# Kernel optimization log

Hardware: AMD Instinct MI355X
Metric: run time of the kernel (lower is better)

The kernel has to match this reference:

```python
import jax, jax.numpy as jnp
import numpy as np

DIM = 192
HEADS = 4
EMBED = 48


def setup_inputs() -> dict:
    key = jax.random.key(0)
    ks = jax.random.split(key, 8)
    b, c, h, w = 8, DIM, 128, 128
    x = jax.random.normal(ks[0], (b, c, h, w), dtype=jnp.float32)
    prior = jax.random.normal(ks[1], (b, 1, EMBED * 4), dtype=jnp.float32)
    # learned params (bias=False)
    w_qkv = jax.random.normal(ks[2], (3 * c, c), dtype=jnp.float32) * (1.0 / np.sqrt(c))
    w_dw = jax.random.normal(ks[3], (3 * c, 1, 3, 3), dtype=jnp.float32) * (1.0 / 3.0)
    w_proj = jax.random.normal(ks[4], (c, c), dtype=jnp.float32) * (1.0 / np.sqrt(c))
    w_kernel = jax.random.normal(ks[5], (2 * c, EMBED * 4), dtype=jnp.float32) * (1.0 / np.sqrt(EMBED * 4))
    temperature = jnp.ones((HEADS, 1, 1), dtype=jnp.float32)
    return {"x": x, "prior": prior, "w_qkv": w_qkv, "w_dw": w_dw,
            "w_proj": w_proj, "w_kernel": w_kernel, "temperature": temperature}


def _mdta(x, prior, w_qkv, w_dw, w_proj, w_kernel, temperature):
    b, c, h, w = x.shape
    # prior modulation: Linear(4*embed -> 2*dim), broadcast over (h,w)
    kv = jnp.einsum('blf,of->blo', prior, w_kernel)[:, 0]        # (b, 2c)
    kv1, kv2 = kv[:, :c], kv[:, c:]
    x = x * kv1[:, :, None, None] + kv2[:, :, None, None]
    # 1x1 conv -> depthwise 3x3 conv
    qkv = jnp.einsum('bchw,oc->bohw', x, w_qkv)                   # (b, 3c, h, w)
    qkv = jax.lax.conv_general_dilated(
        qkv, w_dw, window_strides=(1, 1), padding='SAME',
        dimension_numbers=('NCHW', 'OIHW', 'NCHW'), feature_group_count=3 * c)
    q, k, v = jnp.split(qkv, 3, axis=1)
    ch = c // HEADS
    def heads(t):  # (b, c, h, w) -> (b, head, ch, h*w)
        return t.reshape(b, HEADS, ch, h * w)
    q, k, v = heads(q), heads(k), heads(v)
    # L2 normalize over the (h w) reduction axis
    q = q / jnp.linalg.norm(q, axis=-1, keepdims=True).clip(1e-12)
    k = k / jnp.linalg.norm(k, axis=-1, keepdims=True).clip(1e-12)
    attn = jnp.einsum('bhcn,bhdn->bhcd', q, k) * temperature      # (b, head, ch, ch)
    attn = jax.nn.softmax(attn, axis=-1)
    out = jnp.einsum('bhcd,bhdn->bhcn', attn, v).reshape(b, c, h, w)
    return jnp.einsum('bchw,oc->bohw', out, w_proj)


def reference(x, prior, w_qkv, w_dw, w_proj, w_kernel, temperature):
    return _mdta(x, prior, w_qkv, w_dw, w_proj, w_kernel, temperature)
```

## Files before the change

kernel.cpp:

```cpp
#include <hip/hip_runtime.h>
#include <hip/hip_bf16.h>
#include <stdint.h>

typedef float f32x4 __attribute__((ext_vector_type(4)));
typedef __bf16 bf16x8 __attribute__((ext_vector_type(8)));
typedef __bf16 bf16x2 __attribute__((ext_vector_type(2)));

#define NB 8
#define NC 192
#define NO 576
#define NH 128
#define NWID 128
#define NSP 16384
#define NHEADS 4
#define NCH 48

#define OFF_KV    0u
#define OFF_SSQ   12288u
#define OFF_S     24576u
#define OFF_WB    319488u
#define OFF_M     540672u
#define OFF_QKV2  1130496u
#define OFF_QKV1  152125440u

__device__ __forceinline__ void g2l16(const void* g, void* l) {
    __builtin_amdgcn_global_load_lds((const __attribute__((address_space(1))) void*)g,
                                     (__attribute__((address_space(3))) void*)l, 16, 0, 0);
}

__global__ void k_kv(const float* __restrict__ prior, const float* __restrict__ w_kernel,
                     float* __restrict__ kv, float* __restrict__ zbase) {
    int t = blockIdx.x * 256 + threadIdx.x;
    for (int i = t; i < 76800; i += 3072) zbase[i] = 0.f;
    if (t >= NB * 384) return;
    int b = t / 384, j = t % 384;
    const float* p = prior + b * NC;
    const float* wk = w_kernel + j * NC;
    float s = 0.f;
    for (int f = 0; f < NC; ++f) s += p[f] * wk[f];
    kv[t] = s;
}

__global__ void k_wcast(const float* __restrict__ w_qkv, __bf16* __restrict__ Wb) {
    int t = blockIdx.x * 256 + threadIdx.x;
    if (t < NO * NC) Wb[t] = (__bf16)w_qkv[t];
}

__global__ __launch_bounds__(256, 2) void k_qkv(const float* __restrict__ x, const float* __restrict__ kv,
                                                const __bf16* __restrict__ Wb, __bf16* __restrict__ qkv1) {
    __shared__ __align__(16) char lds[73728];
    int b = blockIdx.y, n0 = blockIdx.x * 128;
    int t = threadIdx.x;
#pragma unroll
    for (int i = 0; i < 6; ++i) {
        int s = i * 256 + t;
        int r = s / 24, c = s % 24, g = c ^ ((r >> 2) & 7);
        g2l16(Wb + (size_t)r * NC + g * 8, lds + 49152 + s * 16);
    }
    const float* xb = x + (size_t)b * NC * NSP + n0;
    const float* kvb = kv + b * 384;
#pragma unroll 4
    for (int p = 0; p < 24; ++p) {
        int id = p * 256 + t;
        int c = id >> 5, n4 = (id & 31) << 2;
        f32x4 v = *reinterpret_cast<const f32x4*>(xb + (size_t)c * NSP + n4);
        float k1 = kvb[c], k2 = kvb[192 + c];
        int chi = (c >> 3) ^ ((n4 >> 2) & 7);
        int base = chi * 16 + (c & 7) * 2;
#pragma unroll
        for (int j = 0; j < 4; ++j)
            *reinterpret_cast<__bf16*>((char*)lds + (n4 + j) * 384 + base) = (__bf16)(v[j] * k1 + k2);
    }
    asm volatile("s_waitcnt vmcnt(0)" ::: "memory");
    __syncthreads();
    int w = t >> 6, l = t & 63, lr = l & 15, lg = l >> 4;
    bf16x8 bgf[6][2];
#pragma unroll
    for (int ks = 0; ks < 6; ++ks) {
        int c16 = ks * 4 + lg;
#pragma unroll
        for (int nf = 0; nf < 2; ++nf) {
            int r = w * 32 + nf * 16 + lr;
            bgf[ks][nf] = *reinterpret_cast<const bf16x8*>(lds + r * 384 + ((c16 ^ ((r >> 2) & 7)) << 4));
        }
    }
    for (int ot = 0; ot < 9; ++ot) {
        f32x4 acc[4][2] = {};
#pragma unroll
        for (int ks = 0; ks < 6; ++ks) {
            int c16 = ks * 4 + lg;
            bf16x8 a[4];
#pragma unroll
            for (int mf = 0; mf < 4; ++mf) {
                int r = mf * 16 + lr;
                a[mf] = *reinterpret_cast<const bf16x8*>(lds + 49152 + r * 384 + ((c16 ^ ((r >> 2) & 7)) << 4));
            }
#pragma unroll
            for (int mf = 0; mf < 4; ++mf)
#pragma unroll
                for (int nf = 0; nf < 2; ++nf)
                    acc[mf][nf] = __builtin_amdgcn_mfma_f32_16x16x32_bf16(a[mf], bgf[ks][nf], acc[mf][nf], 0, 0, 0);
        }
        __syncthreads();
        if (ot < 8) {
            const __bf16* asrc = Wb + (size_t)(ot + 1) * 64 * NC;
#pragma unroll
            for (int i = 0; i < 6; ++i) {
                int s = i * 256 + t;
                int r = s / 24, c = s % 24, g = c ^ ((r >> 2) & 7);
                g2l16(asrc + (size_t)r * NC + g * 8, lds + 49152 + s * 16);
            }
        }
        int o0 = ot * 64;
#pragma unroll
        for (int mf = 0; mf < 4; ++mf)
#pragma unroll
            for (int rr = 0; rr < 4; ++rr) {
                int orow = o0 + mf * 16 + lg * 4 + rr;
#pragma unroll
                for (int nf = 0; nf < 2; ++nf)
                    qkv1[(size_t)(b * NO + orow) * NSP + n0 + w * 32 + nf * 16 + lr] = (__bf16)acc[mf][nf][rr];
            }
        if (ot < 8) {
            asm volatile("s_waitcnt vmcnt(32)" ::: "memory");
            __syncthreads();
        }
    }
}

__global__ __launch_bounds__(256) void k_dw(const __bf16* __restrict__ qkv1, const float* __restrict__ w_dw,
                                            __bf16* __restrict__ qkv2, float* __restrict__ ssq) {
    int task = blockIdx.x * 4 + (threadIdx.x >> 6);
    int l = threadIdx.x & 63;
    int strip = task & 7;
    int bo = task >> 3;
    int o = bo % NO, b = bo / NO;
    const __bf16* src = qkv1 + (size_t)bo * NSP;
    __bf16* dst = qkv2 + (size_t)bo * NSP;
    float wd[9];
#pragma unroll
    for (int i = 0; i < 9; ++i) wd[i] = w_dw[o * 9 + i];
    int ys = strip * 16;
    float a0, b0, L0, R0, a1, b1, L1, R1, a2, b2, L2, R2;

#define LOADROW(Y, A, B, L_, R_) {                                            \
        bf16x2 p = {};                                                        \
        int y_ = (Y);                                                         \
        if (y_ >= 0 && y_ < NH) p = *reinterpret_cast<const bf16x2*>(src + y_ * NWID + 2 * l); \
        A = (float)p[0]; B = (float)p[1];                                     \
        L_ = __shfl(B, l - 1); R_ = __shfl(A, l + 1);                         \
        if (l == 0) L_ = 0.f;                                                 \
        if (l == 63) R_ = 0.f; }

    LOADROW(ys - 1, a0, b0, L0, R0)
    LOADROW(ys,     a1, b1, L1, R1)
    float ss = 0.f;
    bool qk = (o < 384);
#pragma unroll 4
    for (int i = 0; i < 16; ++i) {
        LOADROW(ys + i + 1, a2, b2, L2, R2)
        float oa = L0 * wd[0] + a0 * wd[1] + b0 * wd[2]
                 + L1 * wd[3] + a1 * wd[4] + b1 * wd[5]
                 + L2 * wd[6] + a2 * wd[7] + b2 * wd[8];
        float ob = a0 * wd[0] + b0 * wd[1] + R0 * wd[2]
                 + a1 * wd[3] + b1 * wd[4] + R1 * wd[5]
                 + a2 * wd[6] + b2 * wd[7] + R2 * wd[8];
        bf16x2 ov; ov[0] = (__bf16)oa; ov[1] = (__bf16)ob;
        *reinterpret_cast<bf16x2*>(dst + (ys + i) * NWID + 2 * l) = ov;
        if (qk) { float fa = (float)ov[0], fb = (float)ov[1]; ss += fa * fa + fb * fb; }
        a0 = a1; b0 = b1; L0 = L1; R0 = R1;
        a1 = a2; b1 = b2; L1 = L2; R1 = R2;
    }
#undef LOADROW
    if (qk) {
        for (int off = 32; off > 0; off >>= 1) ss += __shfl_down(ss, off);
        if (l == 0) atomicAdd(&ssq[b * 384 + o], ss);
    }
}

__global__ __launch_bounds__(256, 3) void k_sdot(const __bf16* __restrict__ qkv2, float* __restrict__ S) {
    __shared__ __align__(16) char lds[49152];
    int b = blockIdx.z, h = blockIdx.y, n0 = blockIdx.x * 512;
    int t = threadIdx.x;
    int w = t >> 6, l = t & 63, lr = l & 15, lg = l >> 4;
    const __bf16* qsrc = qkv2 + (size_t)(b * NO + h * NCH) * NSP + n0;
    const __bf16* ksrc = qkv2 + (size_t)(b * NO + 192 + h * NCH) * NSP + n0;
    f32x4 acc[3][3] = {};
    for (int pass = 0; pass < 2; ++pass) {
        if (pass) __syncthreads();
        int coff = pass * 256;
#pragma unroll
        for (int i = 0; i < 6; ++i) {
            int s = i * 256 + t;
            int r = s >> 5, c = s & 31, g = c ^ (r & 7);
            g2l16(qsrc + (size_t)r * NSP + coff + g * 8, lds + s * 16);
        }
#pragma unroll
        for (int i = 0; i < 6; ++i) {
            int s = i * 256 + t;
            int r = s >> 5, c = s & 31, g = c ^ (r & 7);
            g2l16(ksrc + (size_t)r * NSP + coff + g * 8, lds + 24576 + s * 16);
        }
        asm volatile("s_waitcnt vmcnt(0)" ::: "memory");
        __syncthreads();
#pragma unroll
        for (int j = 0; j < 2; ++j) {
            int c16 = (w * 2 + j) * 4 + lg;
            bf16x8 a[3], bb[3];
#pragma unroll
            for (int mf = 0; mf < 3; ++mf) {
                int r = mf * 16 + lr;
                a[mf] = *reinterpret_cast<const bf16x8*>(lds + r * 512 + ((c16 ^ (r & 7)) << 4));
            }
#pragma unroll
            for (int nf = 0; nf < 3; ++nf) {
                int r = nf * 16 + lr;
                bb[nf] = *reinterpret_cast<const bf16x8*>(lds + 24576 + r * 512 + ((c16 ^ (r & 7)) << 4));
            }
#pragma unroll
            for (int mf = 0; mf < 3; ++mf)
#pragma unroll
                for (int nf = 0; nf < 3; ++nf)
                    acc[mf][nf] = __builtin_amdgcn_mfma_f32_16x16x32_bf16(a[mf], bb[nf], acc[mf][nf], 0, 0, 0);
        }
    }
    __syncthreads();
    float* red = (float*)lds;
#pragma unroll
    for (int mf = 0; mf < 3; ++mf)
#pragma unroll
        for (int nf = 0; nf < 3; ++nf)
#pragma unroll
            for (int r = 0; r < 4; ++r) {
                int c = mf * 16 + lg * 4 + r, d = nf * 16 + lr;
                red[(w * 48 + c) * 49 + d] = acc[mf][nf][r];
            }
    __syncthreads();
    float* Sb = S + (size_t)(b * NHEADS + h) * NCH * NCH;
    for (int i = 0; i < 9; ++i) {
        int idx = t + i * 256;
        int c = idx / 48, d = idx % 48;
        float s = red[c * 49 + d] + red[(48 + c) * 49 + d] + red[(96 + c) * 49 + d] + red[(144 + c) * 49 + d];
        atomicAdd(&Sb[c * 48 + d], s);
    }
}

__global__ __launch_bounds__(256) void k_soft(const float* __restrict__ S, const float* __restrict__ ssq,
                                              const float* __restrict__ temp, const float* __restrict__ w_proj,
                                              __bf16* __restrict__ M) {
    int b = blockIdx.x / NHEADS, h = blockIdx.x % NHEADS;
    int tid = threadIdx.x;
    __shared__ float attn[48][48];
    __shared__ float inv[96];
    if (tid < 96) {
        int c = tid % 48;
        int isK = tid / 48;
        float v = ssq[b * 384 + isK * 192 + h * NCH + c];
        float nrm = fmaxf(sqrtf(v), 1e-12f);
        inv[tid] = 1.f / nrm;
    }
    __syncthreads();
    float tp = temp[h];
    const float* Sb = S + (size_t)(b * NHEADS + h) * NCH * NCH;
    for (int i = 0; i < 9; ++i) {
        int idx = tid + i * 256;
        int c = idx / 48, d = idx % 48;
        attn[c][d] = Sb[c * 48 + d] * inv[c] * inv[48 + d] * tp;
    }
    __syncthreads();
    if (tid < 48) {
        float m = -1e30f;
        for (int d = 0; d < 48; ++d) m = fmaxf(m, attn[tid][d]);
        float sum = 0.f;
        for (int d = 0; d < 48; ++d) { float e = __expf(attn[tid][d] - m); attn[tid][d] = e; sum += e; }
        float r = 1.f / sum;
        for (int d = 0; d < 48; ++d) attn[tid][d] *= r;
    }
    __syncthreads();
    for (int i = 0; i < 36; ++i) {
        int idx = tid + i * 256;
        int oo = idx / 48, d = idx % 48;
        const float* wp = w_proj + oo * NC + h * NCH;
        float s = 0.f;
        for (int c = 0; c < 48; ++c) s += wp[c] * attn[c][d];
        M[(size_t)(b * NC + oo) * NC + h * NCH + d] = (__bf16)s;
    }
}

__global__ __launch_bounds__(256, 2) void k_out(const __bf16* __restrict__ Mw, const __bf16* __restrict__ qkv2,
                                                float* __restrict__ outp) {
    __shared__ __align__(16) char lds[73728];
    int b = blockIdx.y, n0 = blockIdx.x * 128;
    int t = threadIdx.x;
    const __bf16* asrc0 = Mw + (size_t)(b * NC) * NC;
#pragma unroll
    for (int i = 0; i < 6; ++i) {
        int s = i * 256 + t;
        int r = s / 24, c = s % 24, g = c ^ ((r >> 2) & 7);
        g2l16(asrc0 + (size_t)r * NC + g * 8, lds + 49152 + s * 16);
    }
    const __bf16* vb = qkv2 + (size_t)(b * NO + 384) * NSP + n0;
#pragma unroll 2
    for (int p = 0; p < 12; ++p) {
        int id = p * 256 + t;
        int c = id >> 4, n8 = (id & 15) << 3;
        bf16x8 vv = *reinterpret_cast<const bf16x8*>(vb + (size_t)c * NSP + n8);
        int cb = c >> 3, cl = (c & 7) * 2;
#pragma unroll
        for (int j = 0; j < 8; ++j) {
            int n = n8 + j;
            int chi = cb ^ ((n >> 2) & 7);
            *reinterpret_cast<__bf16*>((char*)lds + n * 384 + chi * 16 + cl) = vv[j];
        }
    }
    asm volatile("s_waitcnt vmcnt(0)" ::: "memory");
    __syncthreads();
    int w = t >> 6, l = t & 63, lr = l & 15, lg = l >> 4;
    bf16x8 bgf[6][2];
#pragma unroll
    for (int ks = 0; ks < 6; ++ks) {
        int c16 = ks * 4 + lg;
#pragma unroll
        for (int nf = 0; nf < 2; ++nf) {
            int r = w * 32 + nf * 16 + lr;
            bgf[ks][nf] = *reinterpret_cast<const bf16x8*>(lds + r * 384 + ((c16 ^ ((r >> 2) & 7)) << 4));
        }
    }
    for (int ot = 0; ot < 3; ++ot) {
        f32x4 acc[4][2] = {};
#pragma unroll
        for (int ks = 0; ks < 6; ++ks) {
            int c16 = ks * 4 + lg;
            bf16x8 a[4];
#pragma unroll
            for (int mf = 0; mf < 4; ++mf) {
                int r = mf * 16 + lr;
                a[mf] = *reinterpret_cast<const bf16x8*>(lds + 49152 + r * 384 + ((c16 ^ ((r >> 2) & 7)) << 4));
            }
#pragma unroll
            for (int mf = 0; mf < 4; ++mf)
#pragma unroll
                for (int nf = 0; nf < 2; ++nf)
                    acc[mf][nf] = __builtin_amdgcn_mfma_f32_16x16x32_bf16(a[mf], bgf[ks][nf], acc[mf][nf], 0, 0, 0);
        }
        __syncthreads();
        if (ot < 2) {
            const __bf16* asrc = Mw + (size_t)(b * NC + (ot + 1) * 64) * NC;
#pragma unroll
            for (int i = 0; i < 6; ++i) {
                int s = i * 256 + t;
                int r = s / 24, c = s % 24, g = c ^ ((r >> 2) & 7);
                g2l16(asrc + (size_t)r * NC + g * 8, lds + 49152 + s * 16);
            }
        }
        int o0 = ot * 64;
#pragma unroll
        for (int mf = 0; mf < 4; ++mf)
#pragma unroll
            for (int rr = 0; rr < 4; ++rr) {
                int orow = o0 + mf * 16 + lg * 4 + rr;
#pragma unroll
                for (int nf = 0; nf < 2; ++nf)
                    outp[(size_t)(b * NC + orow) * NSP + n0 + w * 32 + nf * 16 + lr] = acc[mf][nf][rr];
            }
        if (ot < 2) {
            asm volatile("s_waitcnt vmcnt(32)" ::: "memory");
            __syncthreads();
        }
    }
}

extern "C" void kernel_launch(void* const* d_in, const int* in_sizes, int n_in,
                              void* d_out, int out_size, void* d_ws, size_t ws_size,
                              hipStream_t stream) {
    const float* x        = (const float*)d_in[0];
    const float* prior    = (const float*)d_in[1];
    const float* w_qkv    = (const float*)d_in[2];
    const float* w_dw     = (const float*)d_in[3];
    const float* w_proj   = (const float*)d_in[4];
    const float* w_kernel = (const float*)d_in[5];
    const float* temp     = (const float*)d_in[6];
    char* ws = (char*)d_ws;
    float*  kv    = (float*)(ws + OFF_KV);
    float*  ssq   = (float*)(ws + OFF_SSQ);
    float*  S     = (float*)(ws + OFF_S);
    __bf16* Wb    = (__bf16*)(ws + OFF_WB);
    __bf16* M     = (__bf16*)(ws + OFF_M);
    __bf16* qkv2  = (__bf16*)(ws + OFF_QKV2);
    __bf16* qkv1  = (__bf16*)(ws + OFF_QKV1);
    float*  outp  = (float*)d_out;

    k_kv<<<12, 256, 0, stream>>>(prior, w_kernel, kv, (float*)(ws + OFF_SSQ));
    k_wcast<<<432, 256, 0, stream>>>(w_qkv, Wb);
    k_qkv<<<dim3(128, 8), 256, 0, stream>>>(x, kv, Wb, qkv1);
    k_dw<<<9216, 256, 0, stream>>>(qkv1, w_dw, qkv2, ssq);
    k_sdot<<<dim3(32, 4, 8), 256, 0, stream>>>(qkv2, S);
    k_soft<<<32, 256, 0, stream>>>(S, ssq, temp, w_proj, M);
    k_out<<<dim3(128, 8), 256, 0, stream>>>(M, qkv2, outp);
}
```

Before: 233.9 us.

## Double-buffer weight tiles in QKV GEMM and refine LDS swizzle

The QKV projection kernel now walks the weights in 32-row tiles with two LDS buffers, issuing the next tile's async global-to-LDS load before computing the current one. This replaces the old single-buffer 64-row scheme, which had to wait before refilling. The LDS XOR swizzle becomes ((r ^ r>>2) & 7) in both GEMM kernels to cut bank conflicts. The output kernel's V staging switches to narrower 4-element loads with per-element swizzle. Smaller tiles mean less MFMA work per barrier and more loop iterations.

```diff
diff --git a/kernel.cpp b/kernel.cpp
--- a/kernel.cpp
+++ b/kernel.cpp
@@ -4,6 +4,7 @@
 
 typedef float f32x4 __attribute__((ext_vector_type(4)));
 typedef __bf16 bf16x8 __attribute__((ext_vector_type(8)));
+typedef __bf16 bf16x4 __attribute__((ext_vector_type(4)));
 typedef __bf16 bf16x2 __attribute__((ext_vector_type(2)));
 
 #define NB 8
@@ -22,6 +23,8 @@
 #define OFF_M     540672u
 #define OFF_QKV2  1130496u
 #define OFF_QKV1  152125440u
+
+#define GR(r) (((r) ^ ((r) >> 2)) & 7)
 
 __device__ __forceinline__ void g2l16(const void* g, void* l) {
     __builtin_amdgcn_global_load_lds((const __attribute__((address_space(1))) void*)g,
@@ -52,9 +55,9 @@
     int b = blockIdx.y, n0 = blockIdx.x * 128;
     int t = threadIdx.x;
 #pragma unroll
-    for (int i = 0; i < 6; ++i) {
+    for (int i = 0; i < 3; ++i) {
         int s = i * 256 + t;
-        int r = s / 24, c = s % 24, g = c ^ ((r >> 2) & 7);
+        int r = s / 24, c = s % 24, g = c ^ GR(r);
         g2l16(Wb + (size_t)r * NC + g * 8, lds + 49152 + s * 16);
     }
     const float* xb = x + (size_t)b * NC * NSP + n0;
@@ -65,11 +68,12 @@
         int c = id >> 5, n4 = (id & 31) << 2;
         f32x4 v = *reinterpret_cast<const f32x4*>(xb + (size_t)c * NSP + n4);
         float k1 = kvb[c], k2 = kvb[192 + c];
-        int chi = (c >> 3) ^ ((n4 >> 2) & 7);
-        int base = chi * 16 + (c & 7) * 2;
-#pragma unroll
-        for (int j = 0; j < 4; ++j)
-            *reinterpret_cast<__bf16*>((char*)lds + (n4 + j) * 384 + base) = (__bf16)(v[j] * k1 + k2);
+#pragma unroll
+        for (int j = 0; j < 4; ++j) {
+            int n = n4 + j;
+            int chi = (c >> 3) ^ GR(n);
+            *reinterpret_cast<__bf16*>((char*)lds + n * 384 + chi * 16 + (c & 7) * 2) = (__bf16)(v[j] * k1 + k2);
+        }
     }
     asm volatile("s_waitcnt vmcnt(0)" ::: "memory");
     __syncthreads();
@@ -81,39 +85,39 @@
 #pragma unroll
         for (int nf = 0; nf < 2; ++nf) {
             int r = w * 32 + nf * 16 + lr;
-            bgf[ks][nf] = *reinterpret_cast<const bf16x8*>(lds + r * 384 + ((c16 ^ ((r >> 2) & 7)) << 4));
-        }
-    }
-    for (int ot = 0; ot < 9; ++ot) {
-        f32x4 acc[4][2] = {};
+            bgf[ks][nf] = *reinterpret_cast<const bf16x8*>(lds + r * 384 + ((c16 ^ GR(r)) << 4));
+        }
+    }
+    for (int p = 0; p < 18; ++p) {
+        int cur = p & 1;
+        if (p < 17) {
+            const __bf16* asrc = Wb + (size_t)(p + 1) * 32 * NC;
+#pragma unroll
+            for (int i = 0; i < 3; ++i) {
+                int s = i * 256 + t;
+                int r = s / 24, c = s % 24, g = c ^ GR(r);
+                g2l16(asrc + (size_t)r * NC + g * 8, lds + 49152 + (cur ^ 1) * 12288 + s * 16);
+            }
+        }
+        f32x4 acc[2][2] = {};
 #pragma unroll
         for (int ks = 0; ks < 6; ++ks) {
             int c16 = ks * 4 + lg;
-            bf16x8 a[4];
-#pragma unroll
-            for (int mf = 0; mf < 4; ++mf) {
+            bf16x8 a[2];
+#pragma unroll
+            for (int mf = 0; mf < 2; ++mf) {
                 int r = mf * 16 + lr;
-                a[mf] = *reinterpret_cast<const bf16x8*>(lds + 49152 + r * 384 + ((c16 ^ ((r >> 2) & 7)) << 4));
-            }
-#pragma unroll
-            for (int mf = 0; mf < 4; ++mf)
+                a[mf] = *reinterpret_cast<const bf16x8*>(lds + 49152 + cur * 12288 + r * 384 + ((c16 ^ GR(r)) << 4));
+            }
+#pragma unroll
+            for (int mf = 0; mf < 2; ++mf)
 #pragma unroll
                 for (int nf = 0; nf < 2; ++nf)
                     acc[mf][nf] = __builtin_amdgcn_mfma_f32_16x16x32_bf16(a[mf], bgf[ks][nf], acc[mf][nf], 0, 0, 0);
         }
-        __syncthreads();
-        if (ot < 8) {
-            const __bf16* asrc = Wb + (size_t)(ot + 1) * 64 * NC;
-#pragma unroll
-            for (int i = 0; i < 6; ++i) {
-                int s = i * 256 + t;
-                int r = s / 24, c = s % 24, g = c ^ ((r >> 2) & 7);
-                g2l16(asrc + (size_t)r * NC + g * 8, lds + 49152 + s * 16);
-            }
-        }
-        int o0 = ot * 64;
-#pragma unroll
-        for (int mf = 0; mf < 4; ++mf)
+        int o0 = p * 32;
+#pragma unroll
+        for (int mf = 0; mf < 2; ++mf)
 #pragma unroll
             for (int rr = 0; rr < 4; ++rr) {
                 int orow = o0 + mf * 16 + lg * 4 + rr;
@@ -121,8 +125,8 @@
                 for (int nf = 0; nf < 2; ++nf)
                     qkv1[(size_t)(b * NO + orow) * NSP + n0 + w * 32 + nf * 16 + lr] = (__bf16)acc[mf][nf][rr];
             }
-        if (ot < 8) {
-            asm volatile("s_waitcnt vmcnt(32)" ::: "memory");
+        if (p < 17) {
+            asm volatile("s_waitcnt vmcnt(16)" ::: "memory");
             __syncthreads();
         }
     }
@@ -296,21 +300,20 @@
 #pragma unroll
     for (int i = 0; i < 6; ++i) {
         int s = i * 256 + t;
-        int r = s / 24, c = s % 24, g = c ^ ((r >> 2) & 7);
+        int r = s / 24, c = s % 24, g = c ^ GR(r);
         g2l16(asrc0 + (size_t)r * NC + g * 8, lds + 49152 + s * 16);
     }
     const __bf16* vb = qkv2 + (size_t)(b * NO + 384) * NSP + n0;
-#pragma unroll 2
-    for (int p = 0; p < 12; ++p) {
+#pragma unroll 4
+    for (int p = 0; p < 24; ++p) {
         int id = p * 256 + t;
-        int c = id >> 4, n8 = (id & 15) << 3;
-        bf16x8 vv = *reinterpret_cast<const bf16x8*>(vb + (size_t)c * NSP + n8);
-        int cb = c >> 3, cl = (c & 7) * 2;
-#pragma unroll
-        for (int j = 0; j < 8; ++j) {
-            int n = n8 + j;
-            int chi = cb ^ ((n >> 2) & 7);
-            *reinterpret_cast<__bf16*>((char*)lds + n * 384 + chi * 16 + cl) = vv[j];
+        int c = id >> 5, n4 = (id & 31) << 2;
+        bf16x4 vv = *reinterpret_cast<const bf16x4*>(vb + (size_t)c * NSP + n4);
+#pragma unroll
+        for (int j = 0; j < 4; ++j) {
+            int n = n4 + j;
+            int chi = (c >> 3) ^ GR(n);
+            *reinterpret_cast<__bf16*>((char*)lds + n * 384 + chi * 16 + (c & 7) * 2) = vv[j];
         }
     }
     asm volatile("s_waitcnt vmcnt(0)" ::: "memory");
@@ -323,7 +326,7 @@
 #pragma unroll
         for (int nf = 0; nf < 2; ++nf) {
             int r = w * 32 + nf * 16 + lr;
-            bgf[ks][nf] = *reinterpret_cast<const bf16x8*>(lds + r * 384 + ((c16 ^ ((r >> 2) & 7)) << 4));
+            bgf[ks][nf] = *reinterpret_cast<const bf16x8*>(lds + r * 384 + ((c16 ^ GR(r)) << 4));
         }
     }
     for (int ot = 0; ot < 3; ++ot) {
@@ -335,7 +338,7 @@
 #pragma unroll
             for (int mf = 0; mf < 4; ++mf) {
                 int r = mf * 16 + lr;
-                a[mf] = *reinterpret_cast<const bf16x8*>(lds + 49152 + r * 384 + ((c16 ^ ((r >> 2) & 7)) << 4));
+                a[mf] = *reinterpret_cast<const bf16x8*>(lds + 49152 + r * 384 + ((c16 ^ GR(r)) << 4));
             }
 #pragma unroll
             for (int mf = 0; mf < 4; ++mf)
@@ -349,7 +352,7 @@
 #pragma unroll
             for (int i = 0; i < 6; ++i) {
                 int s = i * 256 + t;
-                int r = s / 24, c = s % 24, g = c ^ ((r >> 2) & 7);
+                int r = s / 24, c = s % 24, g = c ^ GR(r);
                 g2l16(asrc + (size_t)r * NC + g * 8, lds + 49152 + s * 16);
             }
         }
```

Result: faster. 227.8 us (-2.6%).
